# Kernel optimization log

Measured on AMD Instinct MI355X. Metric: run time of the kernel, lower is better.

The kernel has to match this reference:

```python
import jax, jax.numpy as jnp
import numpy as np

NEG_INF = -9e15
LEAKY_SLOPE = 0.01  # torch F.leaky_relu default


def setup_inputs() -> dict:
    key = jax.random.key(0)
    k1, k2, k3, k4 = jax.random.split(key, 4)
    N, F = 8192, 128
    inp = jax.random.normal(k1, (N, F), dtype=jnp.float32)
    adj = jax.random.randint(k2, (N, N), 0, 2, dtype=jnp.int32)
    # xavier_uniform with gain=1.414
    gain = 1.414
    limW = gain * np.sqrt(6.0 / (F + F))
    W = jax.random.uniform(k3, (F, F), minval=-limW, maxval=limW, dtype=jnp.float32)
    lima = gain * np.sqrt(6.0 / (2 * F + 1))
    a = jax.random.uniform(k4, (2 * F, 1), minval=-lima, maxval=lima, dtype=jnp.float32)
    return {"input": inp, "adj": adj, "W": W, "a": a}


def reference(input, adj, W, a):
    F_ = W.shape[0]
    h = input @ W                               # [N, F]
    # a_input[i,j] = concat(h[i], h[j]); (a_input @ a)[i,j] = h[i]@a1 + h[j]@a2
    a1, a2 = a[:F_, 0], a[F_:, 0]               # [F], [F]
    s1 = h @ a1                                 # [N]
    s2 = h @ a2                                 # [N]
    e = jax.nn.leaky_relu(s1[:, None] + s2[None, :], negative_slope=LEAKY_SLOPE)  # [N, N]
    masked = jnp.where(adj > 0, e, jnp.float32(NEG_INF))
    attention = jax.nn.softmax(masked, axis=1)  # [N, N]
    return attention @ h                        # [N, F]
```

## Files before the change

kernel.cpp:

```cpp
#include <hip/hip_runtime.h>
#include <hip/hip_bf16.h>

#define NN 8192
#define FF 128

typedef unsigned short ushort_t;
typedef __attribute__((ext_vector_type(4))) float f32x4;
typedef __attribute__((ext_vector_type(8))) short s16x8;

__device__ __forceinline__ void block_sync_lds() {
  asm volatile("s_waitcnt lgkmcnt(0)\n\ts_barrier" ::: "memory");
}

__global__ __launch_bounds__(256)
void k1_hw(const float* __restrict__ inp, const float* __restrict__ W,
           const float* __restrict__ a, ushort_t* __restrict__ hT,
           float* __restrict__ s1g, float* __restrict__ Ug, float* __restrict__ Vg)
{
  __shared__ float Wl[FF * FF];
  __shared__ float il[32 * 129];
  __shared__ float red1[32 * 8];
  __shared__ float red2[32 * 8];
  const int t = threadIdx.x;
  const int ib = blockIdx.x * 32;

  {
    const float4* Ws = (const float4*)W;
    float4* Wd = (float4*)Wl;
#pragma unroll
    for (int q = 0; q < 16; ++q) Wd[t + 256 * q] = Ws[t + 256 * q];
  }
#pragma unroll
  for (int q = 0; q < 4; ++q) {
    int idx = t + 256 * q;
    int r = idx >> 5, c4 = idx & 31;
    float4 v = ((const float4*)(inp + (size_t)(ib + r) * FF))[c4];
    float* dst = &il[r * 129 + c4 * 4];
    dst[0] = v.x; dst[1] = v.y; dst[2] = v.z; dst[3] = v.w;
  }
  __syncthreads();

  const int r = t & 31;
  const int c0 = (t >> 5) * 16;
  float acc[16];
#pragma unroll
  for (int j = 0; j < 16; ++j) acc[j] = 0.f;

#pragma unroll 4
  for (int k = 0; k < FF; ++k) {
    float iv = il[r * 129 + k];
    const float4* wrow = (const float4*)&Wl[k * FF + c0];
    float4 w0 = wrow[0], w1 = wrow[1], w2 = wrow[2], w3 = wrow[3];
    acc[0]  += iv * w0.x; acc[1]  += iv * w0.y; acc[2]  += iv * w0.z; acc[3]  += iv * w0.w;
    acc[4]  += iv * w1.x; acc[5]  += iv * w1.y; acc[6]  += iv * w1.z; acc[7]  += iv * w1.w;
    acc[8]  += iv * w2.x; acc[9]  += iv * w2.y; acc[10] += iv * w2.z; acc[11] += iv * w2.w;
    acc[12] += iv * w3.x; acc[13] += iv * w3.y; acc[14] += iv * w3.z; acc[15] += iv * w3.w;
  }

  float ps1 = 0.f, ps2 = 0.f;
#pragma unroll
  for (int q = 0; q < 4; ++q) {
    float4 a1v = *(const float4*)(a + c0 + 4 * q);
    float4 a2v = *(const float4*)(a + FF + c0 + 4 * q);
    ps1 += acc[4*q+0]*a1v.x + acc[4*q+1]*a1v.y + acc[4*q+2]*a1v.z + acc[4*q+3]*a1v.w;
    ps2 += acc[4*q+0]*a2v.x + acc[4*q+1]*a2v.y + acc[4*q+2]*a2v.z + acc[4*q+3]*a2v.w;
  }
  red1[r * 8 + (t >> 5)] = ps1;
  red2[r * 8 + (t >> 5)] = ps2;

#pragma unroll
  for (int j = 0; j < 16; ++j) {
    unsigned b = __float_as_uint(acc[j]);
    hT[(unsigned)(c0 + j) * NN + (unsigned)(ib + r)] = (ushort_t)((b + 0x8000u) >> 16);
  }
  __syncthreads();
  if (t < 32) {
    float s1 = 0.f, s2 = 0.f;
#pragma unroll
    for (int g2 = 0; g2 < 8; ++g2) { s1 += red1[t * 8 + g2]; s2 += red2[t * 8 + g2]; }
    s1g[ib + t] = s1;
    Ug[ib + t] = expf(s2);
    Vg[ib + t] = expf(0.01f * s2);
  }
}

__global__ __launch_bounds__(256)
void k3_attn(const int* __restrict__ adj, const float* __restrict__ s1g,
             const float* __restrict__ Ug, const float* __restrict__ Vg,
             const ushort_t* __restrict__ hT, float* __restrict__ out)
{
  __shared__ ushort_t htl[2][64 * FF];
  __shared__ ushort_t wl[2][32 * 64];
  __shared__ float zl[32];

  const int t = threadIdx.x;
  const int ib = blockIdx.x * 32;
  const int sj = t & 15, g = t >> 4;
  const int lane = t & 63, wv = t >> 6;
  const int wr = wv >> 1, wc = wv & 1;
  const int kidx = lane >> 4;
  const int arow = wr * 16 + (lane & 15);
  const int colbase = wc * 64 + (lane & 15);
  const int c_st = wv * 32 + (lane >> 3);
  const int slot_st = lane & 7;

  const float s1a = s1g[ib + g], s1b = s1g[ib + g + 16];
  const float la = s1a > 0.f ? s1a : 0.01f * s1a;
  const float lb = s1b > 0.f ? s1b : 0.01f * s1b;
  const float Pa = expf(s1a - la - 24.f), Qa = expf(0.01f * s1a - la - 24.f), Ea = expf(-s1a);
  const float Pb = expf(s1b - lb - 24.f), Qb = expf(0.01f * s1b - lb - 24.f), Eb = expf(-s1b);

  float z0 = 0.f, z1 = 0.f;
  f32x4 acc[4];
#pragma unroll
  for (int n = 0; n < 4; ++n) { acc[n][0] = 0.f; acc[n][1] = 0.f; acc[n][2] = 0.f; acc[n][3] = 0.f; }

  const int4* adjr0 = (const int4*)(adj + (size_t)(ib + g) * NN);
  const int4* adjr1 = (const int4*)(adj + (size_t)(ib + g + 16) * NN);
  const float4* Up = (const float4*)Ug;
  const float4* Vp = (const float4*)Vg;
  const ushort_t* hbase = hT + (size_t)c_st * NN + slot_st * 8;

  struct TileRegs { int4 A0, A1; float4 U4, V4; s16x8 H0, H1, H2, H3; };

  auto loadT = [&](TileRegs& R, int js) {
    const int i4 = js * 16 + sj;
    R.A0 = adjr0[i4];
    R.A1 = adjr1[i4];
    R.U4 = Up[i4];
    R.V4 = Vp[i4];
    const ushort_t* hs = hbase + js * 64;
    R.H0 = *(const s16x8*)(hs);
    R.H1 = *(const s16x8*)(hs + 8 * NN);
    R.H2 = *(const s16x8*)(hs + 16 * NN);
    R.H3 = *(const s16x8*)(hs + 24 * NN);
  };

  auto wquad = [&](const int4& A, const float4& Uv, const float4& Vv,
                   float P, float Q, float E, float& z) -> uint2 {
    float w0 = Uv.x > E ? P * Uv.x : Q * Vv.x;  w0 = A.x > 0 ? w0 : 0.f;
    float w1 = Uv.y > E ? P * Uv.y : Q * Vv.y;  w1 = A.y > 0 ? w1 : 0.f;
    float w2 = Uv.z > E ? P * Uv.z : Q * Vv.z;  w2 = A.z > 0 ? w2 : 0.f;
    float w3 = Uv.w > E ? P * Uv.w : Q * Vv.w;  w3 = A.w > 0 ? w3 : 0.f;
    z += (w0 + w1) + (w2 + w3);
    unsigned p0 = ((__float_as_uint(w0) + 0x8000u) >> 16) | ((__float_as_uint(w1) + 0x8000u) & 0xFFFF0000u);
    unsigned p1 = ((__float_as_uint(w2) + 0x8000u) >> 16) | ((__float_as_uint(w3) + 0x8000u) & 0xFFFF0000u);
    return make_uint2(p0, p1);
  };

  auto storeT = [&](int buf, const TileRegs& R) {
    char* hb = (char*)htl[buf] + c_st * 128 + ((slot_st ^ (c_st & 7)) << 4);
    *(s16x8*)(hb)            = R.H0;
    *(s16x8*)(hb + 8 * 128)  = R.H1;
    *(s16x8*)(hb + 16 * 128) = R.H2;
    *(s16x8*)(hb + 24 * 128) = R.H3;
    uint2 pa = wquad(R.A0, R.U4, R.V4, Pa, Qa, Ea, z0);
    uint2 pb = wquad(R.A1, R.U4, R.V4, Pb, Qb, Eb, z1);
    char* wb = (char*)wl[buf] + (((sj >> 1) ^ (g & 7)) << 4) + ((sj & 1) << 3);
    *(uint2*)(wb + g * 128)        = pa;
    *(uint2*)(wb + (g + 16) * 128) = pb;
  };

  auto domfma = [&](int buf) {
    const char* wb = (const char*)wl[buf];
    const char* hb = (const char*)htl[buf];
#pragma unroll
    for (int s = 0; s < 2; ++s) {
      const int kslot = s * 4 + kidx;
      s16x8 af = *(const s16x8*)(wb + arow * 128 + ((kslot ^ (arow & 7)) << 4));
#pragma unroll
      for (int n = 0; n < 4; ++n) {
        const int col = colbase + n * 16;
        s16x8 bf = *(const s16x8*)(hb + col * 128 + ((kslot ^ (col & 7)) << 4));
        acc[n] = __builtin_amdgcn_mfma_f32_16x16x32_bf16(af, bf, acc[n], 0, 0, 0);
      }
    }
  };

  TileRegs RA, RB;
  loadT(RA, 0);
  storeT(0, RA);
  loadT(RA, 1);
  loadT(RB, 2);
  block_sync_lds();

  for (int js = 0; js < 128; js += 2) {
    storeT(1, RA);
    if (js + 3 < 128) loadT(RA, js + 3);
    domfma(0);
    block_sync_lds();
    if (js + 2 < 128) storeT(0, RB);
    if (js + 4 < 128) loadT(RB, js + 4);
    domfma(1);
    block_sync_lds();
  }

#pragma unroll
  for (int m = 1; m < 16; m <<= 1) {
    z0 += __shfl_xor(z0, m);
    z1 += __shfl_xor(z1, m);
  }
  if (sj == 0) { zl[g] = 1.f / z0; zl[g + 16] = 1.f / z1; }
  __syncthreads();

#pragma unroll
  for (int n = 0; n < 4; ++n) {
    const int col = colbase + n * 16;
#pragma unroll
    for (int r2 = 0; r2 < 4; ++r2) {
      const int row = wr * 16 + kidx * 4 + r2;
      out[(size_t)(ib + row) * FF + col] = acc[n][r2] * zl[row];
    }
  }
}

extern "C" void kernel_launch(void* const* d_in, const int* in_sizes, int n_in,
                              void* d_out, int out_size, void* d_ws, size_t ws_size,
                              hipStream_t stream)
{
  const float* inp = (const float*)d_in[0];
  const int* adj   = (const int*)d_in[1];
  const float* W   = (const float*)d_in[2];
  const float* a   = (const float*)d_in[3];
  float* out = (float*)d_out;

  char* ws = (char*)d_ws;
  ushort_t* hT = (ushort_t*)ws;
  float* s1g = (float*)(ws + (size_t)(2u << 20));
  float* Ug  = (float*)(ws + (size_t)(2u << 20) + (32u << 10));
  float* Vg  = (float*)(ws + (size_t)(2u << 20) + (64u << 10));

  hipLaunchKernelGGL(k1_hw, dim3(256), dim3(256), 0, stream, inp, W, a, hT, s1g, Ug, Vg);
  hipLaunchKernelGGL(k3_attn, dim3(256), dim3(256), 0, stream, adj, s1g, Ug, Vg, hT, out);
}
```

Measured before the change: 437.3 us.

## Split attention K dimension across waves, load MFMA operands directly from global

Restructures the attention kernel so each block handles 16 rows with 8 waves, and each wave covers its own 1024-column slice of the neighbour dimension (split-K). Each wave builds the weight fragment in registers and loads the bf16 h fragments straight from global memory, with no LDS staging or per-tile barriers. Partial accumulators and softmax denominators are reduced across waves through LDS at the end. Adjacency is read with nontemporal loads. This removes the LDS double-buffer pipeline and its synchronisation and adds parallelism (512 blocks of 512 threads). In exchange, global h loads are less coalesced and h is re-read by every block, and there is extra reduction traffic at the end.

Result: slower. 494.9 us (+13.2%).

```diff
diff --git a/kernel.cpp b/kernel.cpp
--- a/kernel.cpp
+++ b/kernel.cpp
@@ -6,11 +6,8 @@
 
 typedef unsigned short ushort_t;
 typedef __attribute__((ext_vector_type(4))) float f32x4;
+typedef __attribute__((ext_vector_type(4))) int i32x4;
 typedef __attribute__((ext_vector_type(8))) short s16x8;
-
-__device__ __forceinline__ void block_sync_lds() {
-  asm volatile("s_waitcnt lgkmcnt(0)\n\ts_barrier" ::: "memory");
-}
 
 __global__ __launch_bounds__(256)
 void k1_hw(const float* __restrict__ inp, const float* __restrict__ W,
@@ -84,133 +81,95 @@
   }
 }
 
-__global__ __launch_bounds__(256)
+__global__ __launch_bounds__(512, 2)
 void k3_attn(const int* __restrict__ adj, const float* __restrict__ s1g,
              const float* __restrict__ Ug, const float* __restrict__ Vg,
              const ushort_t* __restrict__ hT, float* __restrict__ out)
 {
-  __shared__ ushort_t htl[2][64 * FF];
-  __shared__ ushort_t wl[2][32 * 64];
-  __shared__ float zl[32];
+  __shared__ float accL[8][16][128];
+  __shared__ float zL[8][16];
 
   const int t = threadIdx.x;
-  const int ib = blockIdx.x * 32;
-  const int sj = t & 15, g = t >> 4;
-  const int lane = t & 63, wv = t >> 6;
-  const int wr = wv >> 1, wc = wv & 1;
-  const int kidx = lane >> 4;
-  const int arow = wr * 16 + (lane & 15);
-  const int colbase = wc * 64 + (lane & 15);
-  const int c_st = wv * 32 + (lane >> 3);
-  const int slot_st = lane & 7;
+  const int lane = t & 63, w = t >> 6;
+  const int rowl = lane & 15, kq = lane >> 4;
+  const int rb = blockIdx.x * 16;
+  const int jb = w * 1024 + kq * 8;
 
-  const float s1a = s1g[ib + g], s1b = s1g[ib + g + 16];
-  const float la = s1a > 0.f ? s1a : 0.01f * s1a;
-  const float lb = s1b > 0.f ? s1b : 0.01f * s1b;
-  const float Pa = expf(s1a - la - 24.f), Qa = expf(0.01f * s1a - la - 24.f), Ea = expf(-s1a);
-  const float Pb = expf(s1b - lb - 24.f), Qb = expf(0.01f * s1b - lb - 24.f), Eb = expf(-s1b);
+  const float s1v = s1g[rb + rowl];
+  const float lv = s1v > 0.f ? s1v : 0.01f * s1v;
+  const float P = expf(s1v - lv - 24.f);
+  const float Q = expf(0.01f * s1v - lv - 24.f);
+  const float E = expf(-s1v);
 
-  float z0 = 0.f, z1 = 0.f;
-  f32x4 acc[4];
+  f32x4 acc[8];
 #pragma unroll
-  for (int n = 0; n < 4; ++n) { acc[n][0] = 0.f; acc[n][1] = 0.f; acc[n][2] = 0.f; acc[n][3] = 0.f; }
+  for (int n = 0; n < 8; ++n) { acc[n][0] = 0.f; acc[n][1] = 0.f; acc[n][2] = 0.f; acc[n][3] = 0.f; }
+  float z = 0.f;
 
-  const int4* adjr0 = (const int4*)(adj + (size_t)(ib + g) * NN);
-  const int4* adjr1 = (const int4*)(adj + (size_t)(ib + g + 16) * NN);
-  const float4* Up = (const float4*)Ug;
-  const float4* Vp = (const float4*)Vg;
-  const ushort_t* hbase = hT + (size_t)c_st * NN + slot_st * 8;
+  const i32x4* adjv = (const i32x4*)(adj + (size_t)(rb + rowl) * NN + jb);
+  const float4* Uv = (const float4*)(Ug + jb);
+  const float4* Vv = (const float4*)(Vg + jb);
+  const ushort_t* hp[8];
+#pragma unroll
+  for (int n = 0; n < 8; ++n) hp[n] = hT + (size_t)(n * 16 + rowl) * NN + jb;
 
-  struct TileRegs { int4 A0, A1; float4 U4, V4; s16x8 H0, H1, H2, H3; };
+#pragma unroll 2
+  for (int ks = 0; ks < 32; ++ks) {
+    i32x4 A0 = __builtin_nontemporal_load(adjv + ks * 8);
+    i32x4 A1 = __builtin_nontemporal_load(adjv + ks * 8 + 1);
+    float4 u0 = Uv[ks * 8], u1 = Uv[ks * 8 + 1];
+    float4 v0 = Vv[ks * 8], v1 = Vv[ks * 8 + 1];
 
-  auto loadT = [&](TileRegs& R, int js) {
-    const int i4 = js * 16 + sj;
-    R.A0 = adjr0[i4];
-    R.A1 = adjr1[i4];
-    R.U4 = Up[i4];
-    R.V4 = Vp[i4];
-    const ushort_t* hs = hbase + js * 64;
-    R.H0 = *(const s16x8*)(hs);
-    R.H1 = *(const s16x8*)(hs + 8 * NN);
-    R.H2 = *(const s16x8*)(hs + 16 * NN);
-    R.H3 = *(const s16x8*)(hs + 24 * NN);
-  };
+    float w0 = u0.x > E ? P * u0.x : Q * v0.x;  w0 = A0[0] > 0 ? w0 : 0.f;
+    float w1 = u0.y > E ? P * u0.y : Q * v0.y;  w1 = A0[1] > 0 ? w1 : 0.f;
+    float w2 = u0.z > E ? P * u0.z : Q * v0.z;  w2 = A0[2] > 0 ? w2 : 0.f;
+    float w3 = u0.w > E ? P * u0.w : Q * v0.w;  w3 = A0[3] > 0 ? w3 : 0.f;
+    float w4 = u1.x > E ? P * u1.x : Q * v1.x;  w4 = A1[0] > 0 ? w4 : 0.f;
+    float w5 = u1.y > E ? P * u1.y : Q * v1.y;  w5 = A1[1] > 0 ? w5 : 0.f;
+    float w6 = u1.z > E ? P * u1.z : Q * v1.z;  w6 = A1[2] > 0 ? w6 : 0.f;
+    float w7 = u1.w > E ? P * u1.w : Q * v1.w;  w7 = A1[3] > 0 ? w7 : 0.f;
+    z += ((w0 + w1) + (w2 + w3)) + ((w4 + w5) + (w6 + w7));
 
-  auto wquad = [&](const int4& A, const float4& Uv, const float4& Vv,
-                   float P, float Q, float E, float& z) -> uint2 {
-    float w0 = Uv.x > E ? P * Uv.x : Q * Vv.x;  w0 = A.x > 0 ? w0 : 0.f;
-    float w1 = Uv.y > E ? P * Uv.y : Q * Vv.y;  w1 = A.y > 0 ? w1 : 0.f;
-    float w2 = Uv.z > E ? P * Uv.z : Q * Vv.z;  w2 = A.z > 0 ? w2 : 0.f;
-    float w3 = Uv.w > E ? P * Uv.w : Q * Vv.w;  w3 = A.w > 0 ? w3 : 0.f;
-    z += (w0 + w1) + (w2 + w3);
     unsigned p0 = ((__float_as_uint(w0) + 0x8000u) >> 16) | ((__float_as_uint(w1) + 0x8000u) & 0xFFFF0000u);
     unsigned p1 = ((__float_as_uint(w2) + 0x8000u) >> 16) | ((__float_as_uint(w3) + 0x8000u) & 0xFFFF0000u);
-    return make_uint2(p0, p1);
-  };
+    unsigned p2 = ((__float_as_uint(w4) + 0x8000u) >> 16) | ((__float_as_uint(w5) + 0x8000u) & 0xFFFF0000u);
+    unsigned p3 = ((__float_as_uint(w6) + 0x8000u) >> 16) | ((__float_as_uint(w7) + 0x8000u) & 0xFFFF0000u);
+    union { unsigned u[4]; s16x8 v; } afu;
+    afu.u[0] = p0; afu.u[1] = p1; afu.u[2] = p2; afu.u[3] = p3;
+    s16x8 af = afu.v;
 
-  auto storeT = [&](int buf, const TileRegs& R) {
-    char* hb = (char*)htl[buf] + c_st * 128 + ((slot_st ^ (c_st & 7)) << 4);
-    *(s16x8*)(hb)            = R.H0;
-    *(s16x8*)(hb + 8 * 128)  = R.H1;
-    *(s16x8*)(hb + 16 * 128) = R.H2;
-    *(s16x8*)(hb + 24 * 128) = R.H3;
-    uint2 pa = wquad(R.A0, R.U4, R.V4, Pa, Qa, Ea, z0);
-    uint2 pb = wquad(R.A1, R.U4, R.V4, Pb, Qb, Eb, z1);
-    char* wb = (char*)wl[buf] + (((sj >> 1) ^ (g & 7)) << 4) + ((sj & 1) << 3);
-    *(uint2*)(wb + g * 128)        = pa;
-    *(uint2*)(wb + (g + 16) * 128) = pb;
-  };
-
-  auto domfma = [&](int buf) {
-    const char* wb = (const char*)wl[buf];
-    const char* hb = (const char*)htl[buf];
 #pragma unroll
-    for (int s = 0; s < 2; ++s) {
-      const int kslot = s * 4 + kidx;
-      s16x8 af = *(const s16x8*)(wb + arow * 128 + ((kslot ^ (arow & 7)) << 4));
-#pragma unroll
-      for (int n = 0; n < 4; ++n) {
-        const int col = colbase + n * 16;
-        s16x8 bf = *(const s16x8*)(hb + col * 128 + ((kslot ^ (col & 7)) << 4));
-        acc[n] = __builtin_amdgcn_mfma_f32_16x16x32_bf16(af, bf, acc[n], 0, 0, 0);
-      }
+    for (int n = 0; n < 8; ++n) {
+      s16x8 bf = *(const s16x8*)(hp[n] + ks * 32);
+      acc[n] = __builtin_amdgcn_mfma_f32_16x16x32_bf16(af, bf, acc[n], 0, 0, 0);
     }
-  };
-
-  TileRegs RA, RB;
-  loadT(RA, 0);
-  storeT(0, RA);
-  loadT(RA, 1);
-  loadT(RB, 2);
-  block_sync_lds();
-
-  for (int js = 0; js < 128; js += 2) {
-    storeT(1, RA);
-    if (js + 3 < 128) loadT(RA, js + 3);
-    domfma(0);
-    block_sync_lds();
-    if (js + 2 < 128) storeT(0, RB);
-    if (js + 4 < 128) loadT(RB, js + 4);
-    domfma(1);
-    block_sync_lds();
   }
 
+  z += __shfl_xor(z, 16);
+  z += __shfl_xor(z, 32);
+
 #pragma unroll
-  for (int m = 1; m < 16; m <<= 1) {
-    z0 += __shfl_xor(z0, m);
-    z1 += __shfl_xor(z1, m);
-  }
-  if (sj == 0) { zl[g] = 1.f / z0; zl[g + 16] = 1.f / z1; }
+  for (int n = 0; n < 8; ++n)
+#pragma unroll
+    for (int r2 = 0; r2 < 4; ++r2)
+      accL[w][kq * 4 + r2][n * 16 + rowl] = acc[n][r2];
+  if (lane < 16) zL[w][lane] = z;
   __syncthreads();
 
+  {
+    const int idx = t * 4;
+    const int row = idx >> 7, col = idx & 127;
+    f32x4 s; s[0] = 0.f; s[1] = 0.f; s[2] = 0.f; s[3] = 0.f;
+    float zs = 0.f;
 #pragma unroll
-  for (int n = 0; n < 4; ++n) {
-    const int col = colbase + n * 16;
-#pragma unroll
-    for (int r2 = 0; r2 < 4; ++r2) {
-      const int row = wr * 16 + kidx * 4 + r2;
-      out[(size_t)(ib + row) * FF + col] = acc[n][r2] * zl[row];
+    for (int w2 = 0; w2 < 8; ++w2) {
+      s += *(const f32x4*)&accL[w2][row][col];
+      zs += zL[w2][row];
     }
+    const float rz = 1.f / zs;
+    float4 o;
+    o.x = s[0] * rz; o.y = s[1] * rz; o.z = s[2] * rz; o.w = s[3] * rz;
+    *(float4*)(out + (size_t)(rb + row) * FF + col) = o;
   }
 }
 
@@ -231,5 +190,5 @@
   float* Vg  = (float*)(ws + (size_t)(2u << 20) + (64u << 10));
 
   hipLaunchKernelGGL(k1_hw, dim3(256), dim3(256), 0, stream, inp, W, a, hT, s1g, Ug, Vg);
-  hipLaunchKernelGGL(k3_attn, dim3(256), dim3(256), 0, stream, adj, s1g, Ug, Vg, hT, out);
+  hipLaunchKernelGGL(k3_attn, dim3(512), dim3(512), 0, stream, adj, s1g, Ug, Vg, hT, out);
 }
```
